# Kernel tuning notes

Measured on AMD Instinct MI355X. Metric: run time of the kernel, lower is better.

The kernel has to match this reference:

```python
import jax, jax.numpy as jnp
import numpy as np

B, N, C = 4, 4096, 256
NUM_HEADS = 8
NUM_GROUPS = 4  # num_groups2, recursive_index=True path
HEAD_DIM = C // NUM_HEADS
SCALE = HEAD_DIM ** -0.5


def setup_inputs() -> dict:
    key = jax.random.key(0)
    k_x, k_idx, k_qkv, k_proj, k_pb = jax.random.split(key, 5)
    x = jax.random.normal(k_x, (B, N, C), dtype=jnp.float32)
    idx = jax.random.permutation(k_idx, N)  # random token shuffle (torch.randperm)
    # nn.Linear params (torch convention: y = x @ W.T + b)
    w_qkv = jax.random.normal(k_qkv, (3 * C, C), dtype=jnp.float32) * (1.0 / np.sqrt(C))
    w_proj = jax.random.normal(k_proj, (C, C), dtype=jnp.float32) * (1.0 / np.sqrt(C))
    b_proj = jax.random.normal(k_pb, (C,), dtype=jnp.float32) * 0.01
    return {"x": x, "idx": idx, "w_qkv": w_qkv, "w_proj": w_proj, "b_proj": b_proj}


def reference(x, idx, w_qkv, w_proj, b_proj):
    g, H, d = NUM_GROUPS, NUM_HEADS, HEAD_DIM
    n = N // g  # tokens per group
    inverse = jnp.argsort(idx)
    xp = x[:, idx, :]  # shuffled tokens [B, N, C]
    # qkv projection then split into groups/heads: [B, g, n, 3, H, d]
    qkv = (xp @ w_qkv.T).reshape(B, g, n, 3, H, d)
    q = qkv[:, :, :, 0].transpose(0, 1, 3, 2, 4)  # [B, g, H, n, d]
    k = qkv[:, :, :, 1].transpose(0, 1, 3, 2, 4)
    v = qkv[:, :, :, 2].transpose(0, 1, 3, 2, 4)
    attn = jnp.einsum('bghnd,bghmd->bghnm', q, k) * SCALE  # [B, g, H, n, n]
    attn = jax.nn.softmax(attn, axis=-1)
    o = jnp.einsum('bghnm,bghmd->bghnd', attn, v)
    # [B, g, H, n, d] -> [B, g, n, H, d] -> [B, N, C] (group-major token order)
    o = o.transpose(0, 1, 3, 2, 4).reshape(B, N, C)
    o = o[:, inverse, :]  # undo the shuffle
    return o @ w_proj.T + b_proj
```

## Files before the change

### kernel.cpp

```cpp
#include <hip/hip_runtime.h>
#include <hip/hip_bf16.h>


typedef __attribute__((ext_vector_type(8))) short bf16x8;
typedef __attribute__((ext_vector_type(4))) float f32x4;

__device__ __forceinline__ unsigned short f2bf(float x){
  __hip_bfloat16 h = __float2bfloat16(x);
  return __builtin_bit_cast(unsigned short, h);
}

__device__ __forceinline__ bf16x8 cvt8(const float4 f0, const float4 f1){
  bf16x8 v;
  v[0]=(short)f2bf(f0.x); v[1]=(short)f2bf(f0.y);
  v[2]=(short)f2bf(f0.z); v[3]=(short)f2bf(f0.w);
  v[4]=(short)f2bf(f1.x); v[5]=(short)f2bf(f1.y);
  v[6]=(short)f2bf(f1.z); v[7]=(short)f2bf(f1.w);
  return v;
}

#define QSCALE (0.17677669529663687f * 1.4426950408889634f)


__global__ __launch_bounds__(256, 3) void qkv_gemm(
    const float* __restrict__ x, const int* __restrict__ idx,
    const float* __restrict__ w_qkv,
    unsigned short* __restrict__ Qb, unsigned short* __restrict__ KF,
    unsigned short* __restrict__ VF)
{
  __shared__ __align__(16) unsigned short Asl[128*64];
  __shared__ __align__(16) unsigned short Bsl[128*64];
  const int tid = threadIdx.x;
  const int bx = blockIdx.x, by = blockIdx.y;
  const int m0 = bx << 7;
  const int bb = bx >> 5;
  const int gg = (bx >> 3) & 3;
  const int j0 = (bx & 31) << 7;
  const int n0 = by << 7;

  int srow[2], brow[2], wb[2];
  #pragma unroll
  for (int it = 0; it < 2; ++it){
    int c = (it << 8) + tid;
    int row = c >> 2;
    int k8 = (c & 3) << 3;
    srow[it] = (bb << 12) + idx[j0 + row];
    brow[it] = n0 + row;
    wb[it] = ((row << 7) + (k8 << 1)) ^ ((row & 7) << 4);
  }

  #pragma unroll
  for (int it = 0; it < 2; ++it){
    int k8 = (((it << 8) + tid) & 3) << 3;
    const float* xs = x + srow[it]*256 + k8;
    const float* wsp = w_qkv + brow[it]*256 + k8;
    *(bf16x8*)((char*)Asl + wb[it]) = cvt8(*(const float4*)(xs), *(const float4*)(xs+4));
    *(bf16x8*)((char*)Bsl + wb[it]) = cvt8(*(const float4*)(wsp), *(const float4*)(wsp+4));
  }
  __syncthreads();

  const int lane = tid & 63;
  const int w = tid >> 6, wr = w >> 1, wc = w & 1;
  const int lr = lane & 15, lg = lane >> 4;
  const int ka = lg << 3;

  f32x4 acc[4][4];
  #pragma unroll
  for (int il = 0; il < 4; ++il)
    #pragma unroll
    for (int jl = 0; jl < 4; ++jl)
      acc[il][jl] = (f32x4){0.f,0.f,0.f,0.f};

  for (int st = 0; st < 8; ++st){
    float4 a0[2], a1[2], c0[2], c1[2];
    const bool pf = (st < 7);
    if (pf){
      int kb = (st + 1) << 5;
      #pragma unroll
      for (int it = 0; it < 2; ++it){
        int k8 = (((it << 8) + tid) & 3) << 3;
        const float* xs = x + srow[it]*256 + kb + k8;
        const float* wsp = w_qkv + brow[it]*256 + kb + k8;
        a0[it] = *(const float4*)(xs);  a1[it] = *(const float4*)(xs + 4);
        c0[it] = *(const float4*)(wsp); c1[it] = *(const float4*)(wsp + 4);
      }
    }

    bf16x8 af[4], bfr[4];
    #pragma unroll
    for (int il = 0; il < 4; ++il){
      int rowA = (wr << 6) + (il << 4) + lr;
      af[il] = *(const bf16x8*)((const char*)Asl + (((rowA << 7) + (ka << 1)) ^ ((rowA & 7) << 4)));
      int rowB = (wc << 6) + (il << 4) + lr;
      bfr[il] = *(const bf16x8*)((const char*)Bsl + (((rowB << 7) + (ka << 1)) ^ ((rowB & 7) << 4)));
    }
    __builtin_amdgcn_s_setprio(1);
    #pragma unroll
    for (int il = 0; il < 4; ++il)
      #pragma unroll
      for (int jl = 0; jl < 4; ++jl)
        acc[il][jl] = __builtin_amdgcn_mfma_f32_16x16x32_bf16(af[il], bfr[jl], acc[il][jl], 0, 0, 0);
    __builtin_amdgcn_s_setprio(0);

    __syncthreads();
    if (pf){
      #pragma unroll
      for (int it = 0; it < 2; ++it){
        *(bf16x8*)((char*)Asl + wb[it]) = cvt8(a0[it], a1[it]);
        *(bf16x8*)((char*)Bsl + wb[it]) = cvt8(c0[it], c1[it]);
      }
      __syncthreads();
    }
  }

  const int s = by >> 1;
  const int hbase = ((bb << 2) + gg) << 3;
  #pragma unroll
  for (int il = 0; il < 4; ++il){
    int mr0 = m0 + (wr << 6) + (il << 4) + (lg << 2);
    int nl0 = mr0 & 1023;
    int t   = nl0 >> 5;
    #pragma unroll
    for (int jl = 0; jl < 4; ++jl){
      int ocol = ((by & 1) << 7) + (wc << 6) + (jl << 4) + lr;
      int h  = ocol >> 5, dd = ocol & 31;
      int head = hbase + h;
      if (s == 2){
        int m = nl0 & 31;
        int lane2 = ((m >> 3) << 4) + (dd & 15);
        int half = dd >> 4;
        ushort4 pk;
        pk.x = f2bf(acc[il][jl][0]); pk.y = f2bf(acc[il][jl][1]);
        pk.z = f2bf(acc[il][jl][2]); pk.w = f2bf(acc[il][jl][3]);
        *(ushort4*)(VF + head*32768 + t*1024 + half*512 + lane2*8 + (m & 7)) = pk;
      } else if (s == 1){
        int r0 = nl0 & 31;
        int f  = (r0 >> 2) & 1;
        unsigned short* dst = KF + head*32768 + t*1024 + f*512
                             + ((((dd >> 3) << 4) + ((r0 >> 3) << 2)) << 3) + (dd & 7);
        dst[0]  = f2bf(acc[il][jl][0]);
        dst[8]  = f2bf(acc[il][jl][1]);
        dst[16] = f2bf(acc[il][jl][2]);
        dst[24] = f2bf(acc[il][jl][3]);
      } else {
        unsigned short* dst = Qb + head*32768 + dd;
        #pragma unroll
        for (int q = 0; q < 4; ++q)
          dst[(nl0 + q) << 5] = f2bf(acc[il][jl][q] * QSCALE);
      }
    }
  }
}

__device__ __forceinline__ void softmax16(
    const f32x4 s0, const f32x4 s1, const f32x4 s2, const f32x4 s3,
    bf16x8& pf0, bf16x8& pf1)
{
  float p0=__builtin_amdgcn_exp2f(s0[0]);  float p1=__builtin_amdgcn_exp2f(s0[1]);
  float p2=__builtin_amdgcn_exp2f(s0[2]);  float p3=__builtin_amdgcn_exp2f(s0[3]);
  float p4=__builtin_amdgcn_exp2f(s1[0]);  float p5=__builtin_amdgcn_exp2f(s1[1]);
  float p6=__builtin_amdgcn_exp2f(s1[2]);  float p7=__builtin_amdgcn_exp2f(s1[3]);
  float p8=__builtin_amdgcn_exp2f(s2[0]);  float p9=__builtin_amdgcn_exp2f(s2[1]);
  float p10=__builtin_amdgcn_exp2f(s2[2]); float p11=__builtin_amdgcn_exp2f(s2[3]);
  float p12=__builtin_amdgcn_exp2f(s3[0]); float p13=__builtin_amdgcn_exp2f(s3[1]);
  float p14=__builtin_amdgcn_exp2f(s3[2]); float p15=__builtin_amdgcn_exp2f(s3[3]);

  pf0[0]=(short)f2bf(p0);  pf0[1]=(short)f2bf(p1);
  pf0[2]=(short)f2bf(p2);  pf0[3]=(short)f2bf(p3);
  pf0[4]=(short)f2bf(p4);  pf0[5]=(short)f2bf(p5);
  pf0[6]=(short)f2bf(p6);  pf0[7]=(short)f2bf(p7);
  pf1[0]=(short)f2bf(p8);  pf1[1]=(short)f2bf(p9);
  pf1[2]=(short)f2bf(p10); pf1[3]=(short)f2bf(p11);
  pf1[4]=(short)f2bf(p12); pf1[5]=(short)f2bf(p13);
  pf1[6]=(short)f2bf(p14); pf1[7]=(short)f2bf(p15);
}

__global__ __launch_bounds__(256, 2) void attn_kernel(
    const unsigned short* __restrict__ Qb, const unsigned short* __restrict__ KF,
    const unsigned short* __restrict__ VF, unsigned short* __restrict__ OB)
{
  __shared__ __align__(16) char lds[65536];
  const int tid  = threadIdx.x;
  const int head = blockIdx.x >> 2;
  const int qblk = blockIdx.x & 3;
  const int lane = tid & 63;
  const int w  = tid >> 6;
  const int lr = lane & 15, lg = lane >> 4;
  const int q0 = qblk * 256 + w * 64;

  const unsigned short* kf = KF + head*32768;
  const unsigned short* vf = VF + head*32768;
  const unsigned short* qbase = Qb + head*32768;

  #pragma unroll
  for (int j = 0; j < 4; ++j){
    int c = (j << 8) + tid;
    *(bf16x8*)(lds + c*16)         = *(const bf16x8*)(kf + c*8);
    *(bf16x8*)(lds + 16384 + c*16) = *(const bf16x8*)(vf + c*8);
  }

  bf16x8 qf[4];
  #pragma unroll
  for (int g = 0; g < 4; ++g)
    qf[g] = *(const bf16x8*)(qbase + (q0 + g*16 + lr)*32 + (lg << 3));

  const short one_bf = (short)0x3F80;
  bf16x8 onesf = {one_bf,one_bf,one_bf,one_bf,one_bf,one_bf,one_bf,one_bf};

  f32x4 o0[4], o1[4], ls[4];
  #pragma unroll
  for (int g = 0; g < 4; ++g){
    o0[g] = (f32x4){0.f,0.f,0.f,0.f};
    o1[g] = (f32x4){0.f,0.f,0.f,0.f};
    ls[g] = (f32x4){0.f,0.f,0.f,0.f};
  }
  const f32x4 zz={0.f,0.f,0.f,0.f};

  __syncthreads();
  int cur = 0;
  for (int it = 0; it < 4; ++it){
    bf16x8 kr[4], vr[4];
    const bool pfch = (it < 3);
    if (pfch){
      #pragma unroll
      for (int j = 0; j < 4; ++j){
        int c = (j << 8) + tid;
        kr[j] = *(const bf16x8*)(kf + (it+1)*8192 + c*8);
        vr[j] = *(const bf16x8*)(vf + (it+1)*8192 + c*8);
      }
    }

    const char* KL = lds + cur*32768 + lane*16;
    const char* VL = KL + 16384;
    #pragma unroll
    for (int hh = 0; hh < 4; ++hh){
      const char* kp_ = KL + hh*4096;
      const char* vp_ = VL + hh*4096;
      bf16x8 kA0 = *(const bf16x8*)(kp_);
      bf16x8 kB0 = *(const bf16x8*)(kp_ + 1024);
      bf16x8 kA1 = *(const bf16x8*)(kp_ + 2048);
      bf16x8 kB1 = *(const bf16x8*)(kp_ + 3072);
      bf16x8 v00 = *(const bf16x8*)(vp_);
      bf16x8 v01 = *(const bf16x8*)(vp_ + 1024);
      bf16x8 v10 = *(const bf16x8*)(vp_ + 2048);
      bf16x8 v11 = *(const bf16x8*)(vp_ + 3072);

      __builtin_amdgcn_s_setprio(1);
      f32x4 sA0 = __builtin_amdgcn_mfma_f32_16x16x32_bf16(kA0, qf[0], zz, 0, 0, 0);
      f32x4 sB0 = __builtin_amdgcn_mfma_f32_16x16x32_bf16(kB0, qf[0], zz, 0, 0, 0);
      f32x4 sA1 = __builtin_amdgcn_mfma_f32_16x16x32_bf16(kA1, qf[0], zz, 0, 0, 0);
      f32x4 sB1 = __builtin_amdgcn_mfma_f32_16x16x32_bf16(kB1, qf[0], zz, 0, 0, 0);
      __builtin_amdgcn_s_setprio(0);

      #pragma unroll
      for (int g = 0; g < 4; ++g){
        f32x4 nA0, nB0, nA1, nB1;
        if (g < 3){
          __builtin_amdgcn_s_setprio(1);
          nA0 = __builtin_amdgcn_mfma_f32_16x16x32_bf16(kA0, qf[g+1], zz, 0, 0, 0);
          nB0 = __builtin_amdgcn_mfma_f32_16x16x32_bf16(kB0, qf[g+1], zz, 0, 0, 0);
          nA1 = __builtin_amdgcn_mfma_f32_16x16x32_bf16(kA1, qf[g+1], zz, 0, 0, 0);
          nB1 = __builtin_amdgcn_mfma_f32_16x16x32_bf16(kB1, qf[g+1], zz, 0, 0, 0);
          __builtin_amdgcn_s_setprio(0);
        }
        bf16x8 pf0, pf1;
        softmax16(sA0, sB0, sA1, sB1, pf0, pf1);
        __builtin_amdgcn_s_setprio(1);
        o0[g] = __builtin_amdgcn_mfma_f32_16x16x32_bf16(pf0, v00, o0[g], 0, 0, 0);
        o1[g] = __builtin_amdgcn_mfma_f32_16x16x32_bf16(pf0, v01, o1[g], 0, 0, 0);
        o0[g] = __builtin_amdgcn_mfma_f32_16x16x32_bf16(pf1, v10, o0[g], 0, 0, 0);
        o1[g] = __builtin_amdgcn_mfma_f32_16x16x32_bf16(pf1, v11, o1[g], 0, 0, 0);
        ls[g] = __builtin_amdgcn_mfma_f32_16x16x32_bf16(pf0, onesf, ls[g], 0, 0, 0);
        ls[g] = __builtin_amdgcn_mfma_f32_16x16x32_bf16(pf1, onesf, ls[g], 0, 0, 0);
        __builtin_amdgcn_s_setprio(0);
        if (g < 3){ sA0 = nA0; sB0 = nB0; sA1 = nA1; sB1 = nB1; }
      }
    }

    if (pfch){
      char* db = lds + (cur^1)*32768;
      #pragma unroll
      for (int j = 0; j < 4; ++j){
        int c = (j << 8) + tid;
        *(bf16x8*)(db + c*16)         = kr[j];
        *(bf16x8*)(db + 16384 + c*16) = vr[j];
      }
    }
    __syncthreads();
    cur ^= 1;
  }

  const int bI = head >> 5, gI = (head >> 3) & 3, hI = head & 7;
  unsigned short* obase = OB + (bI*4096 + gI*1024 + q0)*256 + hI*32;
  #pragma unroll
  for (int g = 0; g < 4; ++g){
    #pragma unroll
    for (int q = 0; q < 4; ++q){
      float iv = 1.0f / ls[g][q];
      int r = (g << 4) + (lg << 2) + q;
      obase[r*256 + lr]      = f2bf(o0[g][q] * iv);
      obase[r*256 + 16 + lr] = f2bf(o1[g][q] * iv);
    }
  }
}

__global__ __launch_bounds__(256) void proj_gemm(
    const unsigned short* __restrict__ OB, const float* __restrict__ w_proj,
    const float* __restrict__ b_proj, const int* __restrict__ idx,
    float* __restrict__ out)
{
  __shared__ unsigned short Alds[64*256];
  __shared__ unsigned short Blds[64*256];
  const int tid = threadIdx.x;
  const int m0 = blockIdx.x << 6;
  const int bb = m0 >> 12;

  #pragma unroll
  for (int it = 0; it < 8; ++it){
    int c = (it << 8) + tid;
    int row = c >> 5;
    int k8 = (c & 31) << 3;
    int byt = ((row << 9) + (k8 << 1)) ^ ((row & 7) << 4);
    *(bf16x8*)((char*)Alds + byt) = *(const bf16x8*)(OB + (m0+row)*256 + k8);
  }

  const int w  = tid >> 6, lane = tid & 63;
  const int lr = lane & 15, lg = lane >> 4;
  const int wr = w >> 1,  wc = w & 1;

  for (int nt = 0; nt < 2; ++nt){
    const int n0 = blockIdx.y * 128 + nt * 64;
    __syncthreads();
    #pragma unroll
    for (int it = 0; it < 8; ++it){
      int c = (it << 8) + tid;
      int row = c >> 5;
      int k8 = (c & 31) << 3;
      const float4 f0 = *(const float4*)(w_proj + (n0+row)*256 + k8);
      const float4 f1 = *(const float4*)(w_proj + (n0+row)*256 + k8 + 4);
      bf16x8 v;
      v[0]=(short)f2bf(f0.x); v[1]=(short)f2bf(f0.y);
      v[2]=(short)f2bf(f0.z); v[3]=(short)f2bf(f0.w);
      v[4]=(short)f2bf(f1.x); v[5]=(short)f2bf(f1.y);
      v[6]=(short)f2bf(f1.z); v[7]=(short)f2bf(f1.w);
      int byt = ((row << 9) + (k8 << 1)) ^ ((row & 7) << 4);
      *(bf16x8*)((char*)Blds + byt) = v;
    }
    __syncthreads();

    f32x4 acc[2][2];
    #pragma unroll
    for (int i=0;i<2;++i)
      #pragma unroll
      for (int j=0;j<2;++j)
        acc[i][j] = (f32x4){0.f,0.f,0.f,0.f};

    #pragma unroll
    for (int ks = 0; ks < 8; ++ks){
      bf16x8 af[2], bfr[2];
      int ka = (ks << 5) + (lg << 3);
      #pragma unroll
      for (int i=0;i<2;++i){
        int rowA = (wr << 5) + (i << 4) + lr;
        int bytA = ((rowA << 9) + (ka << 1)) ^ ((rowA & 7) << 4);
        af[i] = *(const bf16x8*)((const char*)Alds + bytA);
        int rowB = (wc << 5) + (i << 4) + lr;
        int bytB = ((rowB << 9) + (ka << 1)) ^ ((rowB & 7) << 4);
        bfr[i] = *(const bf16x8*)((const char*)Blds + bytB);
      }
      #pragma unroll
      for (int i=0;i<2;++i)
        #pragma unroll
        for (int j=0;j<2;++j)
          acc[i][j] = __builtin_amdgcn_mfma_f32_16x16x32_bf16(af[i], bfr[j], acc[i][j], 0, 0, 0);
    }

    #pragma unroll
    for (int i=0;i<2;++i){
      int mr0 = m0 + (wr << 5) + (i << 4) + (lg << 2);
      int rd[4];
      #pragma unroll
      for (int q=0;q<4;++q)
        rd[q] = (bb << 12) + idx[(mr0 + q) & 4095];
      #pragma unroll
      for (int j=0;j<2;++j){
        int o = n0 + (wc << 5) + (j << 4) + lr;
        float bias = b_proj[o];
        #pragma unroll
        for (int q=0;q<4;++q)
          out[rd[q]*256 + o] = acc[i][j][q] + bias;
      }
    }
  }
}

extern "C" void kernel_launch(void* const* d_in, const int* in_sizes, int n_in,
                              void* d_out, int out_size, void* d_ws, size_t ws_size,
                              hipStream_t stream)
{
  const float* x      = (const float*)d_in[0];
  const int*   idx    = (const int*)  d_in[1];
  const float* w_qkv  = (const float*)d_in[2];
  const float* w_proj = (const float*)d_in[3];
  const float* b_proj = (const float*)d_in[4];
  float* out = (float*)d_out;

  char* ws = (char*)d_ws;
  unsigned short* Qb = (unsigned short*)(ws);
  unsigned short* KF = (unsigned short*)(ws + (8u  << 20));
  unsigned short* VF = (unsigned short*)(ws + (16u << 20));
  unsigned short* OB = (unsigned short*)(ws + (24u << 20));

  qkv_gemm<<<dim3(128, 6), 256, 0, stream>>>(x, idx, w_qkv, Qb, KF, VF);
  attn_kernel<<<dim3(512), 256, 0, stream>>>(Qb, KF, VF, OB);
  proj_gemm<<<dim3(256, 2), 256, 0, stream>>>(OB, w_proj, b_proj, idx, out);
}
```

Baseline: 59.47 us.

## Stream K/V tiles into LDS with direct global-to-LDS loads and smaller double buffer

Replaces register-staged K/V prefetch (global load to VGPRs, then store to LDS after compute) with direct global_load_lds transfers into the alternate LDS buffer. Halves the per-iteration tile to 128 keys (8 iterations instead of 4), shrinking LDS from 64KB to 32KB. This frees registers and LDS, which could allow higher occupancy, and removes the explicit LDS write pass. The tradeoff is twice as many block-wide barriers, and it relies on each wave's global_load_lds lane layout matching the previous c*16 addressing.

```diff
diff --git a/kernel.cpp b/kernel.cpp
--- a/kernel.cpp
+++ b/kernel.cpp
@@ -17,6 +17,12 @@
   v[4]=(short)f2bf(f1.x); v[5]=(short)f2bf(f1.y);
   v[6]=(short)f2bf(f1.z); v[7]=(short)f2bf(f1.w);
   return v;
+}
+
+__device__ __forceinline__ void gl_lds16(const unsigned short* g, char* l){
+  __builtin_amdgcn_global_load_lds(
+      (const __attribute__((address_space(1))) void*)g,
+      (__attribute__((address_space(3))) void*)l, 16, 0, 0);
 }
 
 #define QSCALE (0.17677669529663687f * 1.4426950408889634f)
@@ -179,7 +185,7 @@
     const unsigned short* __restrict__ Qb, const unsigned short* __restrict__ KF,
     const unsigned short* __restrict__ VF, unsigned short* __restrict__ OB)
 {
-  __shared__ __align__(16) char lds[65536];
+  __shared__ __align__(16) char lds[32768];
   const int tid  = threadIdx.x;
   const int head = blockIdx.x >> 2;
   const int qblk = blockIdx.x & 3;
@@ -192,11 +198,15 @@
   const unsigned short* vf = VF + head*32768;
   const unsigned short* qbase = Qb + head*32768;
 
-  #pragma unroll
-  for (int j = 0; j < 4; ++j){
-    int c = (j << 8) + tid;
-    *(bf16x8*)(lds + c*16)         = *(const bf16x8*)(kf + c*8);
-    *(bf16x8*)(lds + 16384 + c*16) = *(const bf16x8*)(vf + c*8);
+  {
+    char* wbase = lds + (w << 10);
+    #pragma unroll
+    for (int j = 0; j < 2; ++j){
+      const unsigned short* kg = kf + (((j << 8) + tid) << 3);
+      const unsigned short* vg = vf + (((j << 8) + tid) << 3);
+      gl_lds16(kg, wbase + (j << 12));
+      gl_lds16(vg, wbase + 8192 + (j << 12));
+    }
   }
 
   bf16x8 qf[4];
@@ -218,22 +228,22 @@
 
   __syncthreads();
   int cur = 0;
-  for (int it = 0; it < 4; ++it){
-    bf16x8 kr[4], vr[4];
-    const bool pfch = (it < 3);
-    if (pfch){
-      #pragma unroll
-      for (int j = 0; j < 4; ++j){
-        int c = (j << 8) + tid;
-        kr[j] = *(const bf16x8*)(kf + (it+1)*8192 + c*8);
-        vr[j] = *(const bf16x8*)(vf + (it+1)*8192 + c*8);
-      }
-    }
-
-    const char* KL = lds + cur*32768 + lane*16;
-    const char* VL = KL + 16384;
-    #pragma unroll
-    for (int hh = 0; hh < 4; ++hh){
+  for (int it = 0; it < 8; ++it){
+    if (it < 7){
+      char* db = lds + ((cur^1) << 14) + (w << 10);
+      #pragma unroll
+      for (int j = 0; j < 2; ++j){
+        const unsigned short* kg = kf + (it+1)*4096 + (((j << 8) + tid) << 3);
+        const unsigned short* vg = vf + (it+1)*4096 + (((j << 8) + tid) << 3);
+        gl_lds16(kg, db + (j << 12));
+        gl_lds16(vg, db + 8192 + (j << 12));
+      }
+    }
+
+    const char* KL = lds + (cur << 14) + lane*16;
+    const char* VL = KL + 8192;
+    #pragma unroll
+    for (int hh = 0; hh < 2; ++hh){
       const char* kp_ = KL + hh*4096;
       const char* vp_ = VL + hh*4096;
       bf16x8 kA0 = *(const bf16x8*)(kp_);
@@ -277,15 +287,6 @@
       }
     }
 
-    if (pfch){
-      char* db = lds + (cur^1)*32768;
-      #pragma unroll
-      for (int j = 0; j < 4; ++j){
-        int c = (j << 8) + tid;
-        *(bf16x8*)(db + c*16)         = kr[j];
-        *(bf16x8*)(db + 16384 + c*16) = vr[j];
-      }
-    }
     __syncthreads();
     cur ^= 1;
   }
```

Result: faster. 58.20 us (-2.1%).
